# Optimization experiments

Hardware: AMD Instinct MI355X
Metric: run time of the kernel (lower is better)

## Reference

```python
import jax, jax.numpy as jnp
import numpy as np

B, S, E, NH = 2, 2048, 1024, 16
THETA = 10000.0


def setup_inputs() -> dict:
    key = jax.random.key(0)
    k1, k2 = jax.random.split(key, 2)
    hidden_states = jax.random.normal(k1, (B, S, E), dtype=jnp.float32)
    in_proj_weight = jax.random.normal(k2, (3 * E, E), dtype=jnp.float32) * 0.02
    in_proj_bias = jnp.zeros((3 * E,), dtype=jnp.float32)
    return {
        "hidden_states": hidden_states,
        "in_proj_weight": in_proj_weight,
        "in_proj_bias": in_proj_bias,
        "T": 1,
        "H": 32,
        "W": 64,
    }


def _rope(x, cos, sin):
    # x: [BT, seq, n_heads, head_dim]; cos/sin: [seq, head_dim//2]
    # pairs are consecutive elements (x[2i], x[2i+1]) == complex (re, im)
    xr = x.reshape(x.shape[:-1] + (-1, 2))
    xe, xo = xr[..., 0], xr[..., 1]
    c = cos[None, :, None, :]
    s = sin[None, :, None, :]
    re = xe * c - xo * s
    im = xe * s + xo * c
    return jnp.stack([re, im], axis=-1).reshape(x.shape)


def reference(hidden_states, in_proj_weight, in_proj_bias, T, H, W):
    Bx, Sx, Ex = hidden_states.shape
    hd = Ex // NH
    # fused QKV projection
    qkv = hidden_states @ in_proj_weight.T + in_proj_bias
    q, k, v = jnp.split(qkv, 3, axis=-1)
    # 1D rotary over chunks of length S//T (T=1 -> full sequence)
    seq = Sx // T
    inv_freq = 1.0 / (THETA ** (jnp.arange(0, hd, 2, dtype=jnp.float32) / hd))
    ang = jnp.arange(seq, dtype=jnp.float32)[:, None] * inv_freq  # [seq, hd//2]
    cos, sin = jnp.cos(ang), jnp.sin(ang)
    q = _rope(q.reshape(Bx * T, seq, NH, hd), cos, sin).reshape(Bx, Sx, NH, hd)
    k = _rope(k.reshape(Bx * T, seq, NH, hd), cos, sin).reshape(Bx, Sx, NH, hd)
    v = v.reshape(Bx, Sx, NH, hd)
    # scaled dot-product attention (special_attn encoder path: no out_proj)
    scale = 1.0 / jnp.sqrt(jnp.asarray(hd, dtype=jnp.float32))
    scores = jnp.einsum('bqnd,bknd->bnqk', q, k) * scale
    attn = jax.nn.softmax(scores, axis=-1)
    out = jnp.einsum('bnqk,bknd->bqnd', attn, v)
    return out.reshape(Bx, Sx, Ex)
```

## Files before the change

kernel.cpp:

```cpp
#include <hip/hip_runtime.h>
#include <math.h>

#define BB 2
#define SS 2048
#define EE 1024
#define NHH 16
#define HD 64
#define HD2 32

typedef _Float16 f16x8 __attribute__((ext_vector_type(8)));
typedef __attribute__((ext_vector_type(4))) float f32x4;

static __device__ __forceinline__ unsigned pkh(float a, float b) {
    union { _Float16 h[2]; unsigned u; } v;
    v.h[0] = (_Float16)a; v.h[1] = (_Float16)b;
    return v.u;
}

static __device__ __forceinline__ void dma16(const void* g, void* l) {
    __builtin_amdgcn_global_load_lds(
        (const __attribute__((address_space(1))) unsigned int*)g,
        (__attribute__((address_space(3))) unsigned int*)l,
        16, 0, 0);
}

__global__ __launch_bounds__(256) void rope_table_k(float* __restrict__ ct,
                                                    float* __restrict__ st) {
    int idx = blockIdx.x * 256 + threadIdx.x;
    if (idx >= SS * HD2) return;
    int s = idx >> 5, p = idx & 31;
    double inv = pow(10000.0, -(double)(2 * p) / 64.0);
    double ang = (double)s * inv;
    ct[idx] = (float)cos(ang);
    st[idx] = (float)sin(ang);
}

#define NXCHUNK 524288
#define NWCHUNK 393216
__global__ __launch_bounds__(256) void cvt_k(
    const float* __restrict__ X, const float* __restrict__ W,
    unsigned short* __restrict__ Xh, unsigned short* __restrict__ Wh)
{
    int idx = blockIdx.x * 256 + threadIdx.x;
    const float* src;
    unsigned short* dst;
    int c;
    if (idx < NXCHUNK) { src = X; dst = Xh; c = idx; }
    else               { src = W; dst = Wh; c = idx - NXCHUNK;
                         if (c >= NWCHUNK) return; }
    int l15 = c & 15, q = (c >> 4) & 3, grp = (c >> 6) & 7;
    int kt = (c >> 9) & 31, t = c >> 14;
    int row = t * 128 + grp * 16 + l15;
    int k   = kt * 32 + q * 8;
    float4 v0 = *(const float4*)(src + (size_t)row * EE + k);
    float4 v1 = *(const float4*)(src + (size_t)row * EE + k + 4);
    *(uint4*)(dst + (size_t)c * 8) =
        make_uint4(pkh(v0.x, v0.y), pkh(v0.z, v0.w), pkh(v1.x, v1.y), pkh(v1.z, v1.w));
}

__global__ __launch_bounds__(256, 3) void qkv_mfma_k(
    const unsigned short* __restrict__ Xh, const unsigned short* __restrict__ Wh,
    const float* __restrict__ bias,
    const float* __restrict__ ct, const float* __restrict__ st,
    unsigned short* __restrict__ Qg, unsigned short* __restrict__ Kg,
    unsigned short* __restrict__ Vg)
{
    __shared__ __align__(16) unsigned short Alds[4096];
    __shared__ __align__(16) unsigned short Blds[4096];

    const int tid  = threadIdx.x;
    const int wave = tid >> 6;
    const int lane = tid & 63;
    const int quad = lane >> 4;
    const int l15  = lane & 15;

    const int id    = blockIdx.x;
    const int xcd   = id & 7;
    const int local = id >> 3;
    const int nt    = xcd * 3 + local % 3;
    const int mt    = local / 3;
    const int m0    = mt * 128;
    const int n0b   = nt * 128;

    f32x4 acc[4][4];
#pragma unroll
    for (int mc = 0; mc < 4; mc++)
#pragma unroll
        for (int nc = 0; nc < 4; nc++) acc[mc][nc] = (f32x4){0.f, 0.f, 0.f, 0.f};

    const int mg = (wave >> 1) * 4;
    const int ng = (wave & 1) * 4;

    for (int kt = 0; kt < EE / 32; kt++) {
        __syncthreads();
        {
            const unsigned short* at = Xh + ((size_t)(mt * 32 + kt)) * 4096;
            const unsigned short* bt = Wh + ((size_t)(nt * 32 + kt)) * 4096;
            dma16(at + (size_t)tid * 8,         Alds + tid * 8);
            dma16(at + (size_t)(tid + 256) * 8, Alds + (tid + 256) * 8);
            dma16(bt + (size_t)tid * 8,         Blds + tid * 8);
            dma16(bt + (size_t)(tid + 256) * 8, Blds + (tid + 256) * 8);
        }
        __syncthreads();

        f16x8 Af[4], Bf[4];
#pragma unroll
        for (int mc = 0; mc < 4; mc++)
            Af[mc] = *(const f16x8*)(Alds + ((mg + mc) * 4 + quad) * 128 + l15 * 8);
#pragma unroll
        for (int nc = 0; nc < 4; nc++)
            Bf[nc] = *(const f16x8*)(Blds + ((ng + nc) * 4 + quad) * 128 + l15 * 8);
#pragma unroll
        for (int mc = 0; mc < 4; mc++)
#pragma unroll
            for (int nc = 0; nc < 4; nc++)
                acc[mc][nc] = __builtin_amdgcn_mfma_f32_16x16x32_f16(Af[mc], Bf[nc], acc[mc][nc], 0, 0, 0);
    }

    const int n0w = n0b + (wave & 1) * 64;
    const int m0w = m0 + (wave >> 1) * 64;
    const int sec = n0w >> 10;
    const int h   = (n0w & 1023) >> 6;
    const int bq  = m0w >> 11;
    const size_t abase = (size_t)(bq * NHH + h) * 131072;
    unsigned short* dst = (sec == 0) ? Qg : (sec == 1) ? Kg : Vg;

    float bn[4];
#pragma unroll
    for (int nc = 0; nc < 4; nc++) bn[nc] = bias[n0w + nc * 16 + l15];

    if (sec < 2) {
        const float scq = (sec == 0) ? 0.18033688f : 1.0f;
#pragma unroll
        for (int mc = 0; mc < 4; mc++) {
            int sb = (m0w & 2047) + mc * 16;
#pragma unroll
            for (int nc = 0; nc < 4; nc++) {
                int d = nc * 16 + l15;
                int p = d >> 1;
                int kc_d = d >> 5, quad_a = (d >> 3) & 3, j = d & 7;
#pragma unroll
                for (int rr = 0; rr < 4; rr++) {
                    int srow = sb + quad * 4 + rr;
                    float x = acc[mc][nc][rr] + bn[nc];
                    float xp = __shfl_xor(x, 1);
                    float c = ct[srow * 32 + p], sn = st[srow * 32 + p];
                    float o = ((l15 & 1) == 0) ? (x * c - xp * sn) : (xp * sn + x * c);
                    o *= scq;
                    float op = __shfl_xor(o, 1);
                    if ((l15 & 1) == 0) {
                        unsigned u = pkh(o, op);
                        size_t e = abase +
                            (size_t)((((srow >> 4) * 2 + kc_d) * 4 + quad_a)) * 128 +
                            (srow & 15) * 8 + j;
                        *(unsigned int*)(dst + e) = u;
                    }
                }
            }
        }
    } else {
#pragma unroll
        for (int mc = 0; mc < 4; mc++) {
            int sb = (m0w & 2047) + mc * 16;
            int s32 = sb >> 5;
            int quad_v = ((sb >> 3) + (quad >> 1)) & 3;
            int j0 = (quad & 1) * 4;
#pragma unroll
            for (int nc = 0; nc < 4; nc++) {
                float x0 = acc[mc][nc][0] + bn[nc];
                float x1 = acc[mc][nc][1] + bn[nc];
                float x2 = acc[mc][nc][2] + bn[nc];
                float x3 = acc[mc][nc][3] + bn[nc];
                unsigned u01 = pkh(x0, x1), u23 = pkh(x2, x3);
                size_t e = abase +
                    (size_t)(((s32 * 4 + nc) * 4 + quad_v)) * 128 + l15 * 8 + j0;
                *(uint2*)(dst + e) = make_uint2(u01, u23);
            }
        }
    }
}

__global__ __launch_bounds__(128, 2) void attn_mfma_k(
    const unsigned short* __restrict__ Qg,
    const unsigned short* __restrict__ Kg,
    const unsigned short* __restrict__ Vg,
    float* __restrict__ out)
{
    __shared__ __align__(16) unsigned short Klds[4096];
    __shared__ __align__(16) unsigned short Pbuf[2][1088];

    const int tid  = threadIdx.x;
    const int wave = tid >> 6;
    const int lane = tid & 63;
    const int quad = lane >> 4;
    const int l15  = lane & 15;
    const int id   = blockIdx.x;
    const int bh   = (id & 7) * 4 + ((id >> 3) & 3);
    const int qt   = id >> 5;
    const int b    = bh >> 4, h = bh & 15;
    const int q_wave = qt * 64 + wave * 32;
    const size_t abase = (size_t)bh * 131072;

    f16x8 qf[2][2];
#pragma unroll
    for (int nc = 0; nc < 2; nc++)
#pragma unroll
        for (int kc = 0; kc < 2; kc++)
            qf[nc][kc] = *(const f16x8*)(Qg + abase +
                (size_t)(((((q_wave >> 4) + nc) * 2 + kc) * 4 + quad)) * 128 + l15 * 8);

    f32x4 acc[2][4];
#pragma unroll
    for (int nc = 0; nc < 2; nc++)
#pragma unroll
        for (int dc = 0; dc < 4; dc++) acc[nc][dc] = (f32x4){0.f, 0.f, 0.f, 0.f};
    float mst[2] = {-INFINITY, -INFINITY};
    float lst[2] = {0.f, 0.f};

    const unsigned short* kgb = Kg + abase;
    const unsigned short* vgb = Vg + abase;

    for (int kt = 0; kt < SS / 64; kt++) {
        __syncthreads();
#pragma unroll
        for (int i = 0; i < 4; i++)
            dma16(kgb + (size_t)kt * 4096 + (tid + i * 128) * 8,
                  Klds + (tid + i * 128) * 8);
        __syncthreads();

        const unsigned short* vt = vgb + (size_t)kt * 4096;
        f16x8 vf[4][2];
#pragma unroll
        for (int dc = 0; dc < 4; dc++)
#pragma unroll
            for (int kk2 = 0; kk2 < 2; kk2++)
                vf[dc][kk2] = *(const f16x8*)(vt + (kk2 * 16 + dc * 4 + quad) * 128 + l15 * 8);

        f32x4 stt[2][4];
#pragma unroll
        for (int mc = 0; mc < 4; mc++) {
            f16x8 a0 = *(const f16x8*)(Klds + ((mc * 2 + 0) * 4 + quad) * 128 + l15 * 8);
            f16x8 a1 = *(const f16x8*)(Klds + ((mc * 2 + 1) * 4 + quad) * 128 + l15 * 8);
#pragma unroll
            for (int nc = 0; nc < 2; nc++) {
                f32x4 s = (f32x4){0.f, 0.f, 0.f, 0.f};
                s = __builtin_amdgcn_mfma_f32_16x16x32_f16(a0, qf[nc][0], s, 0, 0, 0);
                s = __builtin_amdgcn_mfma_f32_16x16x32_f16(a1, qf[nc][1], s, 0, 0, 0);
                stt[nc][mc] = s;
            }
        }

#pragma unroll
        for (int nc = 0; nc < 2; nc++) {
            float mt = -INFINITY;
#pragma unroll
            for (int mc = 0; mc < 4; mc++)
#pragma unroll
                for (int rr = 0; rr < 4; rr++) mt = fmaxf(mt, stt[nc][mc][rr]);
            mt = fmaxf(mt, __shfl_xor(mt, 16));
            mt = fmaxf(mt, __shfl_xor(mt, 32));
            float mnew = fmaxf(mst[nc], mt);
            float alpha = __builtin_amdgcn_exp2f(mst[nc] - mnew);
            float p[4][4];
            float ps = 0.f;
#pragma unroll
            for (int mc = 0; mc < 4; mc++)
#pragma unroll
                for (int rr = 0; rr < 4; rr++) {
                    float e = __builtin_amdgcn_exp2f(stt[nc][mc][rr] - mnew);
                    p[mc][rr] = e;
                    ps += e;
                }
            ps += __shfl_xor(ps, 16);
            ps += __shfl_xor(ps, 32);
            lst[nc] = lst[nc] * alpha + ps;
            mst[nc] = mnew;

            float ar[4];
#pragma unroll
            for (int rr = 0; rr < 4; rr++)
                ar[rr] = __shfl(alpha, (lane & 48) + ((lane >> 4) << 2) + rr);
#pragma unroll
            for (int dc = 0; dc < 4; dc++)
#pragma unroll
                for (int rr = 0; rr < 4; rr++) acc[nc][dc][rr] *= ar[rr];

            unsigned short* Pw = Pbuf[wave];
#pragma unroll
            for (int mc = 0; mc < 4; mc++)
#pragma unroll
                for (int pr = 0; pr < 2; pr++) {
                    unsigned u = pkh(p[mc][2 * pr], p[mc][2 * pr + 1]);
                    int kk2 = mc >> 1;
                    int quadp = (mc & 1) * 2 + (quad >> 1);
                    int j = (quad & 1) * 4 + 2 * pr;
                    *(unsigned int*)(Pw + (kk2 * 4 + quadp) * 136 + l15 * 8 + j) = u;
                }
            f16x8 pf[2];
#pragma unroll
            for (int kk2 = 0; kk2 < 2; kk2++)
                pf[kk2] = *(const f16x8*)(Pw + (kk2 * 4 + quad) * 136 + l15 * 8);

#pragma unroll
            for (int dc = 0; dc < 4; dc++) {
                f32x4 aa = acc[nc][dc];
#pragma unroll
                for (int kk2 = 0; kk2 < 2; kk2++)
                    aa = __builtin_amdgcn_mfma_f32_16x16x32_f16(pf[kk2], vf[dc][kk2], aa, 0, 0, 0);
                acc[nc][dc] = aa;
            }
        }
    }

#pragma unroll
    for (int nc = 0; nc < 2; nc++) {
        float linv = 1.f / lst[nc];
        float lr[4];
#pragma unroll
        for (int rr = 0; rr < 4; rr++)
            lr[rr] = __shfl(linv, (lane & 48) + ((lane >> 4) << 2) + rr);
#pragma unroll
        for (int dc = 0; dc < 4; dc++)
#pragma unroll
            for (int rr = 0; rr < 4; rr++) {
                int s = q_wave + nc * 16 + quad * 4 + rr;
                out[((size_t)(b * SS + s)) * EE + h * HD + dc * 16 + l15] = acc[nc][dc][rr] * lr[rr];
            }
    }
}

extern "C" void kernel_launch(void* const* d_in, const int* in_sizes, int n_in,
                              void* d_out, int out_size, void* d_ws, size_t ws_size,
                              hipStream_t stream) {
    const float* X    = (const float*)d_in[0];
    const float* W    = (const float*)d_in[1];
    const float* bias = (const float*)d_in[2];
    float* out = (float*)d_out;

    float* ws = (float*)d_ws;
    float* ct = ws;
    float* st = ws + 65536;
    unsigned short* base = (unsigned short*)(ws + 131072);
    const size_t ASZ = (size_t)32 * 131072;
    unsigned short* Qg = base;
    unsigned short* Kg = base + ASZ;
    unsigned short* Vg = base + 2 * ASZ;
    unsigned short* Xh = base + 3 * ASZ;
    unsigned short* Wh = Xh + (size_t)NXCHUNK * 8;

    rope_table_k<<<(SS * HD2 + 255) / 256, 256, 0, stream>>>(ct, st);
    cvt_k<<<(NXCHUNK + NWCHUNK) / 256, 256, 0, stream>>>(X, W, Xh, Wh);
    qkv_mfma_k<<<dim3(768), 256, 0, stream>>>(
        Xh, Wh, bias, ct, st, Qg, Kg, Vg);
    attn_mfma_k<<<dim3(1024), 128, 0, stream>>>(Qg, Kg, Vg, out);
}
```

Before: 192.1 us.

## Double-buffer K tiles, use 4 waves of 16 queries, lazy softmax rescale

Restructures the attention kernel so each block runs 4 waves, each owning 16 query rows instead of 2 waves with 32 rows. K tiles are double-buffered in LDS with the next tile's DMA issued before computing the current one, which cuts one barrier per iteration. The online-softmax rescale is skipped unless the running max grows by more than a threshold, and setprio is placed around the MFMA sections. The padding on the P buffer is removed, which may introduce LDS bank conflicts, and per-wave K reuse drops because each wave now handles fewer query rows.

```diff
diff --git a/kernel.cpp b/kernel.cpp
--- a/kernel.cpp
+++ b/kernel.cpp
@@ -180,14 +180,14 @@
     }
 }
 
-__global__ __launch_bounds__(128, 2) void attn_mfma_k(
+__global__ __launch_bounds__(256, 4) void attn_mfma_k(
     const unsigned short* __restrict__ Qg,
     const unsigned short* __restrict__ Kg,
     const unsigned short* __restrict__ Vg,
     float* __restrict__ out)
 {
-    __shared__ __align__(16) unsigned short Klds[4096];
-    __shared__ __align__(16) unsigned short Pbuf[2][1088];
+    __shared__ __align__(16) unsigned short Klds[2][4096];
+    __shared__ __align__(16) unsigned short Pbuf[4][1024];
 
     const int tid  = threadIdx.x;
     const int wave = tid >> 6;
@@ -198,35 +198,35 @@
     const int bh   = (id & 7) * 4 + ((id >> 3) & 3);
     const int qt   = id >> 5;
     const int b    = bh >> 4, h = bh & 15;
-    const int q_wave = qt * 64 + wave * 32;
+    const int q0   = qt * 64 + wave * 16;
     const size_t abase = (size_t)bh * 131072;
 
-    f16x8 qf[2][2];
-#pragma unroll
-    for (int nc = 0; nc < 2; nc++)
-#pragma unroll
-        for (int kc = 0; kc < 2; kc++)
-            qf[nc][kc] = *(const f16x8*)(Qg + abase +
-                (size_t)(((((q_wave >> 4) + nc) * 2 + kc) * 4 + quad)) * 128 + l15 * 8);
-
-    f32x4 acc[2][4];
-#pragma unroll
-    for (int nc = 0; nc < 2; nc++)
-#pragma unroll
-        for (int dc = 0; dc < 4; dc++) acc[nc][dc] = (f32x4){0.f, 0.f, 0.f, 0.f};
-    float mst[2] = {-INFINITY, -INFINITY};
-    float lst[2] = {0.f, 0.f};
+    f16x8 qf[2];
+#pragma unroll
+    for (int kc = 0; kc < 2; kc++)
+        qf[kc] = *(const f16x8*)(Qg + abase +
+            (size_t)((((q0 >> 4) * 2 + kc) * 4 + quad)) * 128 + l15 * 8);
+
+    f32x4 acc[4];
+#pragma unroll
+    for (int dc = 0; dc < 4; dc++) acc[dc] = (f32x4){0.f, 0.f, 0.f, 0.f};
+    float mst = -INFINITY, lst = 0.f;
 
     const unsigned short* kgb = Kg + abase;
     const unsigned short* vgb = Vg + abase;
-
+    unsigned short* Pw = Pbuf[wave];
+
+    dma16(kgb + (size_t)tid * 8,         &Klds[0][tid * 8]);
+    dma16(kgb + (size_t)(tid + 256) * 8, &Klds[0][(tid + 256) * 8]);
+    __syncthreads();
+
+    int cur = 0;
     for (int kt = 0; kt < SS / 64; kt++) {
-        __syncthreads();
-#pragma unroll
-        for (int i = 0; i < 4; i++)
-            dma16(kgb + (size_t)kt * 4096 + (tid + i * 128) * 8,
-                  Klds + (tid + i * 128) * 8);
-        __syncthreads();
+        if (kt + 1 < SS / 64) {
+            const unsigned short* ks = kgb + (size_t)(kt + 1) * 4096;
+            dma16(ks + (size_t)tid * 8,         &Klds[cur ^ 1][tid * 8]);
+            dma16(ks + (size_t)(tid + 256) * 8, &Klds[cur ^ 1][(tid + 256) * 8]);
+        }
 
         const unsigned short* vt = vgb + (size_t)kt * 4096;
         f16x8 vf[4][2];
@@ -236,46 +236,31 @@
             for (int kk2 = 0; kk2 < 2; kk2++)
                 vf[dc][kk2] = *(const f16x8*)(vt + (kk2 * 16 + dc * 4 + quad) * 128 + l15 * 8);
 
-        f32x4 stt[2][4];
+        f32x4 stt[4];
+        __builtin_amdgcn_s_setprio(1);
 #pragma unroll
         for (int mc = 0; mc < 4; mc++) {
-            f16x8 a0 = *(const f16x8*)(Klds + ((mc * 2 + 0) * 4 + quad) * 128 + l15 * 8);
-            f16x8 a1 = *(const f16x8*)(Klds + ((mc * 2 + 1) * 4 + quad) * 128 + l15 * 8);
-#pragma unroll
-            for (int nc = 0; nc < 2; nc++) {
-                f32x4 s = (f32x4){0.f, 0.f, 0.f, 0.f};
-                s = __builtin_amdgcn_mfma_f32_16x16x32_f16(a0, qf[nc][0], s, 0, 0, 0);
-                s = __builtin_amdgcn_mfma_f32_16x16x32_f16(a1, qf[nc][1], s, 0, 0, 0);
-                stt[nc][mc] = s;
-            }
-        }
-
-#pragma unroll
-        for (int nc = 0; nc < 2; nc++) {
-            float mt = -INFINITY;
-#pragma unroll
-            for (int mc = 0; mc < 4; mc++)
-#pragma unroll
-                for (int rr = 0; rr < 4; rr++) mt = fmaxf(mt, stt[nc][mc][rr]);
-            mt = fmaxf(mt, __shfl_xor(mt, 16));
-            mt = fmaxf(mt, __shfl_xor(mt, 32));
-            float mnew = fmaxf(mst[nc], mt);
-            float alpha = __builtin_amdgcn_exp2f(mst[nc] - mnew);
-            float p[4][4];
-            float ps = 0.f;
-#pragma unroll
-            for (int mc = 0; mc < 4; mc++)
-#pragma unroll
-                for (int rr = 0; rr < 4; rr++) {
-                    float e = __builtin_amdgcn_exp2f(stt[nc][mc][rr] - mnew);
-                    p[mc][rr] = e;
-                    ps += e;
-                }
-            ps += __shfl_xor(ps, 16);
-            ps += __shfl_xor(ps, 32);
-            lst[nc] = lst[nc] * alpha + ps;
-            mst[nc] = mnew;
-
+            f16x8 a0 = *(const f16x8*)(&Klds[cur][((mc * 2 + 0) * 4 + quad) * 128 + l15 * 8]);
+            f16x8 a1 = *(const f16x8*)(&Klds[cur][((mc * 2 + 1) * 4 + quad) * 128 + l15 * 8]);
+            f32x4 s = (f32x4){0.f, 0.f, 0.f, 0.f};
+            s = __builtin_amdgcn_mfma_f32_16x16x32_f16(a0, qf[0], s, 0, 0, 0);
+            s = __builtin_amdgcn_mfma_f32_16x16x32_f16(a1, qf[1], s, 0, 0, 0);
+            stt[mc] = s;
+        }
+        __builtin_amdgcn_s_setprio(0);
+
+        float mt = -INFINITY;
+#pragma unroll
+        for (int mc = 0; mc < 4; mc++)
+#pragma unroll
+            for (int rr = 0; rr < 4; rr++) mt = fmaxf(mt, stt[mc][rr]);
+        mt = fmaxf(mt, __shfl_xor(mt, 16));
+        mt = fmaxf(mt, __shfl_xor(mt, 32));
+
+        if (!__all(mt - mst <= 8.f)) {
+            float mnew = fmaxf(mst, mt);
+            float alpha = __builtin_amdgcn_exp2f(mst - mnew);
+            lst *= alpha;
             float ar[4];
 #pragma unroll
             for (int rr = 0; rr < 4; rr++)
@@ -283,50 +268,60 @@
 #pragma unroll
             for (int dc = 0; dc < 4; dc++)
 #pragma unroll
-                for (int rr = 0; rr < 4; rr++) acc[nc][dc][rr] *= ar[rr];
-
-            unsigned short* Pw = Pbuf[wave];
-#pragma unroll
-            for (int mc = 0; mc < 4; mc++)
-#pragma unroll
-                for (int pr = 0; pr < 2; pr++) {
-                    unsigned u = pkh(p[mc][2 * pr], p[mc][2 * pr + 1]);
-                    int kk2 = mc >> 1;
-                    int quadp = (mc & 1) * 2 + (quad >> 1);
-                    int j = (quad & 1) * 4 + 2 * pr;
-                    *(unsigned int*)(Pw + (kk2 * 4 + quadp) * 136 + l15 * 8 + j) = u;
-                }
-            f16x8 pf[2];
+                for (int rr = 0; rr < 4; rr++) acc[dc][rr] *= ar[rr];
+            mst = mnew;
+        }
+
+        float ps = 0.f;
+#pragma unroll
+        for (int mc = 0; mc < 4; mc++) {
+            float e0 = __builtin_amdgcn_exp2f(stt[mc][0] - mst);
+            float e1 = __builtin_amdgcn_exp2f(stt[mc][1] - mst);
+            float e2 = __builtin_amdgcn_exp2f(stt[mc][2] - mst);
+            float e3 = __builtin_amdgcn_exp2f(stt[mc][3] - mst);
+            ps += (e0 + e1) + (e2 + e3);
+            int kk2 = mc >> 1;
+            int quadp = (mc & 1) * 2 + (quad >> 1);
+            int j0 = (quad & 1) * 4;
+            *(uint2*)(Pw + (kk2 * 4 + quadp) * 128 + l15 * 8 + j0) =
+                make_uint2(pkh(e0, e1), pkh(e2, e3));
+        }
+        ps += __shfl_xor(ps, 16);
+        ps += __shfl_xor(ps, 32);
+        lst += ps;
+
+        f16x8 pf[2];
+#pragma unroll
+        for (int kk2 = 0; kk2 < 2; kk2++)
+            pf[kk2] = *(const f16x8*)(Pw + (kk2 * 4 + quad) * 128 + l15 * 8);
+
+        __builtin_amdgcn_s_setprio(1);
+#pragma unroll
+        for (int dc = 0; dc < 4; dc++) {
+            f32x4 aa = acc[dc];
 #pragma unroll
             for (int kk2 = 0; kk2 < 2; kk2++)
-                pf[kk2] = *(const f16x8*)(Pw + (kk2 * 4 + quad) * 136 + l15 * 8);
-
-#pragma unroll
-            for (int dc = 0; dc < 4; dc++) {
-                f32x4 aa = acc[nc][dc];
-#pragma unroll
-                for (int kk2 = 0; kk2 < 2; kk2++)
-                    aa = __builtin_amdgcn_mfma_f32_16x16x32_f16(pf[kk2], vf[dc][kk2], aa, 0, 0, 0);
-                acc[nc][dc] = aa;
-            }
-        }
+                aa = __builtin_amdgcn_mfma_f32_16x16x32_f16(pf[kk2], vf[dc][kk2], aa, 0, 0, 0);
+            acc[dc] = aa;
+        }
+        __builtin_amdgcn_s_setprio(0);
+
+        __syncthreads();
+        cur ^= 1;
     }
 
-#pragma unroll
-    for (int nc = 0; nc < 2; nc++) {
-        float linv = 1.f / lst[nc];
-        float lr[4];
-#pragma unroll
-        for (int rr = 0; rr < 4; rr++)
-            lr[rr] = __shfl(linv, (lane & 48) + ((lane >> 4) << 2) + rr);
-#pragma unroll
-        for (int dc = 0; dc < 4; dc++)
-#pragma unroll
-            for (int rr = 0; rr < 4; rr++) {
-                int s = q_wave + nc * 16 + quad * 4 + rr;
-                out[((size_t)(b * SS + s)) * EE + h * HD + dc * 16 + l15] = acc[nc][dc][rr] * lr[rr];
-            }
-    }
+    float linv = 1.f / lst;
+    float lr[4];
+#pragma unroll
+    for (int rr = 0; rr < 4; rr++)
+        lr[rr] = __shfl(linv, (lane & 48) + ((lane >> 4) << 2) + rr);
+#pragma unroll
+    for (int dc = 0; dc < 4; dc++)
+#pragma unroll
+        for (int rr = 0; rr < 4; rr++) {
+            int s = q0 + quad * 4 + rr;
+            out[((size_t)(b * SS + s)) * EE + h * HD + dc * 16 + l15] = acc[dc][rr] * lr[rr];
+        }
 }
 
 extern "C" void kernel_launch(void* const* d_in, const int* in_sizes, int n_in,
@@ -352,5 +347,5 @@
     cvt_k<<<(NXCHUNK + NWCHUNK) / 256, 256, 0, stream>>>(X, W, Xh, Wh);
     qkv_mfma_k<<<dim3(768), 256, 0, stream>>>(
         Xh, Wh, bias, ct, st, Qg, Kg, Vg);
-    attn_mfma_k<<<dim3(1024), 128, 0, stream>>>(Qg, Kg, Vg, out);
-}
+    attn_mfma_k<<<dim3(1024), 256, 0, stream>>>(Qg, Kg, Vg, out);
+}
```

Measured after the change: 188.9 us. No clear change (-1.7%).
